# Optimization experiments

Measured on AMD Instinct MI355X. Metric: run time of the kernel, lower is better.

Reference implementation:

```python
import jax, jax.numpy as jnp
import numpy as np

DIM, H, C = 1024, 16, 64
D = DIM // H  # head_dim = 64
GATE_HID = 16


def setup_inputs() -> dict:
    key = jax.random.key(0)
    ks = jax.random.split(key, 8)
    B, L = 2, 2048

    def xav(k, fan_in, fan_out):
        return jax.random.normal(k, (fan_in, fan_out), jnp.float32) * np.sqrt(2.0 / (fan_in + fan_out))

    return {
        "x": jax.random.normal(ks[0], (B, L, DIM), jnp.float32),
        "Wq": xav(ks[1], DIM, DIM), "bq": jnp.zeros((DIM,), jnp.float32),
        "Wk": xav(ks[2], DIM, DIM), "bk": jnp.zeros((DIM,), jnp.float32),
        "Wv": xav(ks[3], DIM, DIM), "bv": jnp.zeros((DIM,), jnp.float32),
        "Wg1": xav(ks[4], DIM, GATE_HID), "bg1": jnp.zeros((GATE_HID,), jnp.float32),
        "Wg2": xav(ks[5], GATE_HID, H * D), "bg2": jnp.zeros((H * D,), jnp.float32),
    }


def reference(x, Wq, bq, Wk, bk, Wv, bv, Wg1, bg1, Wg2, bg2):
    B, L, dim = x.shape
    pad = (-L) % C
    if pad:
        x = jnp.pad(x, ((0, 0), (0, pad), (0, 0)))
    Lp = L + pad

    def proj(W, b):
        # (B, Lp, dim) -> (B, H, Lp, D)
        return (x @ W + b).reshape(B, Lp, H, D).transpose(0, 2, 1, 3)

    q, k, v = proj(Wq, bq), proj(Wk, bk), proj(Wv, bv)
    gate = jax.nn.sigmoid(jax.nn.silu(x @ Wg1 + bg1) @ Wg2 + bg2)
    alpha = 0.9 * gate.reshape(B, Lp, H, D).transpose(0, 2, 1, 3) + 0.1  # (B,H,Lp,D)

    # --- intra-chunk causal softmax attention (vectorized over chunks) ---
    Nc = Lp // C
    qc = q.reshape(B, H, Nc, C, D)
    kc = k.reshape(B, H, Nc, C, D)
    vc = v.reshape(B, H, Nc, C, D)
    scores = jnp.einsum('bhncd,bhnkd->bhnck', qc, kc) / np.sqrt(D).astype(np.float32)
    causal = jnp.tril(jnp.ones((C, C), bool))
    scores = jnp.where(causal, scores, -jnp.inf)
    intra = jnp.einsum('bhnck,bhnke->bhnce', jax.nn.softmax(scores, axis=-1), vc)
    intra = intra.reshape(B, H, Lp, D)

    # --- inter: gated linear-attention recurrence over the full sequence ---
    # Note: in the original code S is updated every timestep (including inside
    # chunks), so the 'inter' term at step t sees ALL tokens < t, not just
    # previous chunks.
    def step(S, inp):
        q_t, k_t, v_t, a_t = inp  # each (B, H, D)
        inter_t = jnp.einsum('bhd,bhde->bhe', q_t, S)
        S = a_t[..., None] * S + k_t[..., None] * v_t[..., None, :]
        return S, inter_t

    xs = tuple(a.transpose(2, 0, 1, 3) for a in (q, k, v, alpha))  # (Lp, B, H, D)
    S0 = jnp.zeros((B, H, D, D), x.dtype)
    _, inter = jax.lax.scan(step, S0, xs)  # (Lp, B, H, D)
    inter = inter.transpose(1, 2, 0, 3)  # (B, H, Lp, D)

    out = (inter + intra).transpose(0, 2, 1, 3).reshape(B, Lp, dim)
    return out[:, :L]
```

## Files before the change

### kernel.cpp

```cpp
#include <hip/hip_runtime.h>
#include <math.h>

#define DIMN 1024
#define NH 16
#define HD 64
#define CHK 64
#define NB 2
#define SEQ 2048
#define NTOK (NB*SEQ)
#define NCHUNK (SEQ/CHK)
#define GH 16

typedef __bf16 bf16x8 __attribute__((ext_vector_type(8)));
typedef float f32x4 __attribute__((ext_vector_type(4)));
typedef unsigned short u16x4 __attribute__((ext_vector_type(4)));

__device__ __forceinline__ unsigned short f2bf(float f) {
  union { float f; unsigned u; } a; a.f = f;
  unsigned r = a.u + 0x7FFFu + ((a.u >> 16) & 1u);
  return (unsigned short)(r >> 16);
}
__device__ __forceinline__ float bf2f(unsigned short v) {
  union { unsigned u; float f; } a; a.u = ((unsigned)v) << 16;
  return a.f;
}

__device__ __forceinline__ void gload16(const void* g, void* l) {
  __builtin_amdgcn_global_load_lds(
      (const __attribute__((address_space(1))) void*)g,
      (__attribute__((address_space(3))) void*)l, 16, 0, 0);
}


__global__ __launch_bounds__(256) void k_cast_x(const float* __restrict__ x,
    unsigned short* __restrict__ xb) {
  size_t i = (size_t)(blockIdx.x*256 + threadIdx.x)*4;
  float4 v = *(const float4*)(x + i);
  ushort4 o;
  o.x = f2bf(v.x); o.y = f2bf(v.y); o.z = f2bf(v.z); o.w = f2bf(v.w);
  *(ushort4*)(xb + i) = o;
}

__global__ __launch_bounds__(256) void k_cast_wT(const float* __restrict__ W0,
    const float* __restrict__ W1, const float* __restrict__ W2,
    unsigned short* __restrict__ wt) {
  __shared__ float tile[64][68];
  int z = blockIdx.z;
  const float* W = z==0 ? W0 : z==1 ? W1 : W2;
  unsigned short* o = wt + (size_t)z*DIMN*DIMN;
  int k0 = blockIdx.y*64, n0 = blockIdx.x*64;
  int tr = threadIdx.x >> 4, c0 = (threadIdx.x & 15)*4;
  #pragma unroll
  for (int s = 0; s < 4; ++s) {
    int r = tr + s*16;
    *(f32x4*)&tile[r][c0] = *(const f32x4*)(W + (size_t)(k0+r)*DIMN + n0 + c0);
  }
  __syncthreads();
  #pragma unroll
  for (int s = 0; s < 4; ++s) {
    int nn = tr + s*16;
    ushort4 v;
    v.x = f2bf(tile[c0+0][nn]);
    v.y = f2bf(tile[c0+1][nn]);
    v.z = f2bf(tile[c0+2][nn]);
    v.w = f2bf(tile[c0+3][nn]);
    *(ushort4*)(o + (size_t)(n0+nn)*DIMN + k0 + c0) = v;
  }
}

__global__ __launch_bounds__(256) void k_wg1t(const float* __restrict__ Wg1,
    unsigned short* __restrict__ wg1b) {
  int idx = blockIdx.x*256 + threadIdx.x;
  int k = idx & 1023, j = idx >> 10;
  wg1b[j*DIMN + k] = f2bf(Wg1[k*GH + j]);
}

__global__ __launch_bounds__(64) void k_hidden(const unsigned short* __restrict__ xb,
    const unsigned short* __restrict__ wg1b, const float* __restrict__ bg1,
    float* __restrict__ hid) {
  int l = threadIdx.x;
  int lr = l & 15, kg = l >> 4;
  int m0 = blockIdx.x * 16;
  union FB { uint4 u; bf16x8 h; } a, b;
  f32x4 acc = {0.f,0.f,0.f,0.f};
  const unsigned short* xrow = xb + (size_t)(m0 + lr)*DIMN + kg*8;
  const unsigned short* wrow = wg1b + (size_t)lr*DIMN + kg*8;
  #pragma unroll 8
  for (int kk = 0; kk < 32; ++kk) {
    a.u = *(const uint4*)(xrow + kk*32);
    b.u = *(const uint4*)(wrow + kk*32);
    acc = __builtin_amdgcn_mfma_f32_16x16x32_bf16(a.h, b.h, acc, 0, 0, 0);
  }
  float bias = bg1[lr];
  #pragma unroll
  for (int rg = 0; rg < 4; ++rg) {
    int m = m0 + kg*4 + rg;
    float v = acc[rg] + bias;
    hid[m*GH + lr] = v / (1.f + expf(-v));
  }
}

__global__ __launch_bounds__(256) void k_projqkv(const unsigned short* __restrict__ xb,
    const unsigned short* __restrict__ wt,
    const float* __restrict__ b0, const float* __restrict__ b1, const float* __restrict__ b2,
    unsigned short* __restrict__ o0, unsigned short* __restrict__ o1,
    unsigned short* __restrict__ o2) {
  __shared__ unsigned short As[2][128*32];
  __shared__ unsigned short Bs[2][128*32];
  int tid = threadIdx.x;
  int n3 = blockIdx.x*128;
  int z = n3 >> 10;
  int n0l = n3 & 1023;
  const float* bias = z==0 ? b0 : z==1 ? b1 : b2;
  unsigned short* out = z==0 ? o0 : z==1 ? o1 : o2;
  int m0 = blockIdx.y*128;

  int l = tid & 63;
  int w = tid >> 6;
  int wr = w >> 1, wc = w & 1;
  int lrow = l & 15, kg = l >> 4;

  f32x4 acc[4][4] = {};

  int r0s = tid >> 2, s0s = tid & 3;
  int r1s = (tid + 256) >> 2;
  int sg0 = s0s ^ ((r0s >> 1) & 3);
  int sg1 = s0s ^ ((r1s >> 1) & 3);

  #define STAGE(buf, kt) do { \
    int kb_ = (kt)*32; \
    gload16(xb + ((size_t)(m0 + r0s)*DIMN + kb_ + sg0*8), &As[buf][tid*8]); \
    gload16(wt + ((size_t)(n3 + r0s)*DIMN + kb_ + sg0*8), &Bs[buf][tid*8]); \
    gload16(xb + ((size_t)(m0 + r1s)*DIMN + kb_ + sg1*8), &As[buf][(tid+256)*8]); \
    gload16(wt + ((size_t)(n3 + r1s)*DIMN + kb_ + sg1*8), &Bs[buf][(tid+256)*8]); \
  } while (0)

  STAGE(0, 0);
  int buf = 0;
  for (int t = 0; t < DIMN/32; ++t) {
    __syncthreads();
    if (t+1 < DIMN/32) STAGE(buf^1, t+1);
    union { uint4 u; bf16x8 h; } af[4], bfr[4];
    #pragma unroll
    for (int mf = 0; mf < 4; ++mf) {
      int r = wr*64 + mf*16 + lrow;
      int slot = kg ^ ((r >> 1) & 3);
      af[mf].u = *(const uint4*)&As[buf][r*32 + slot*8];
    }
    #pragma unroll
    for (int nf = 0; nf < 4; ++nf) {
      int r = wc*64 + nf*16 + lrow;
      int slot = kg ^ ((r >> 1) & 3);
      bfr[nf].u = *(const uint4*)&Bs[buf][r*32 + slot*8];
    }
    #pragma unroll
    for (int mf = 0; mf < 4; ++mf)
      #pragma unroll
      for (int nf = 0; nf < 4; ++nf)
        acc[mf][nf] = __builtin_amdgcn_mfma_f32_16x16x32_bf16(
            af[mf].h, bfr[nf].h, acc[mf][nf], 0, 0, 0);
    buf ^= 1;
  }
  #undef STAGE

  float bv[4];
  #pragma unroll
  for (int nf = 0; nf < 4; ++nf) bv[nf] = bias[n0l + wc*64 + nf*16 + lrow];
  #pragma unroll
  for (int mf = 0; mf < 4; ++mf) {
    int rbase = m0 + wr*64 + mf*16 + kg*4;
    #pragma unroll
    for (int nf = 0; nf < 4; ++nf) {
      int c = n0l + wc*64 + nf*16 + lrow;
      #pragma unroll
      for (int rg = 0; rg < 4; ++rg)
        out[(size_t)(rbase+rg)*DIMN + c] = f2bf(acc[mf][nf][rg] + bv[nf]);
    }
  }
}

__global__ __launch_bounds__(256) void k_ginc(const unsigned short* __restrict__ kbuf,
    const unsigned short* __restrict__ vbuf,
    const float* __restrict__ hid, const float* __restrict__ Wg2,
    const float* __restrict__ bg2,
    float* __restrict__ G, float* __restrict__ Bv) {
  __shared__ __align__(16) float kl[CHK][HD+4];
  __shared__ __align__(16) float vl[CHK][HD+4];
  __shared__ __align__(16) float al[CHK][HD+4];
  __shared__ float wprod[4][HD];
  int tid = threadIdx.x;
  int bid = blockIdx.x;
  int bh = bid >> 5, n = bid & 31;
  int b = bh >> 4, h = bh & 15;
  int colbase = h*HD;
  size_t rowbase = (size_t)b*SEQ + n*CHK;
  int dd = tid & 63, w = tid >> 6;

  float* scr = &al[0][0];
  {
    int r = tid >> 2, j0 = (tid & 3)*4;
    *(f32x4*)&scr[r*16 + j0] = *(const f32x4*)(hid + (rowbase + r)*GH + j0);
    int j = tid >> 4, d0 = (tid & 15)*4;
    *(f32x4*)&scr[1024 + j*64 + d0] = *(const f32x4*)(Wg2 + (size_t)j*DIMN + colbase + d0);
  }
  #pragma unroll
  for (int i = 0; i < 4; ++i) {
    int f4 = tid + i*256;
    int r = f4 >> 4, cg = f4 & 15;
    size_t g = (rowbase + r)*DIMN + colbase + cg*4;
    u16x4 k4 = *(const u16x4*)(kbuf + g);
    u16x4 v4 = *(const u16x4*)(vbuf + g);
    #pragma unroll
    for (int j = 0; j < 4; ++j) {
      kl[r][cg*4+j] = bf2f(k4[j]);
      vl[r][cg*4+j] = bf2f(v4[j]);
    }
  }
  __syncthreads();

  float av[16];
  {
    int r = tid >> 2, db = (tid & 3)*16;
    #pragma unroll
    for (int dq = 0; dq < 16; ++dq) {
      int d = db + dq;
      float acc = bg2[colbase + d];
      #pragma unroll
      for (int j = 0; j < GH; ++j)
        acc = fmaf(scr[r*16 + j], scr[1024 + j*64 + d], acc);
      float gg = 1.f/(1.f + expf(-acc));
      av[dq] = fmaf(0.9f, gg, 0.1f);
    }
  }
  __syncthreads();
  {
    int r = tid >> 2, db = (tid & 3)*16;
    #pragma unroll
    for (int dq = 0; dq < 16; dq += 4) {
      f32x4 v4 = {av[dq], av[dq+1], av[dq+2], av[dq+3]};
      *(f32x4*)&al[r][db + dq] = v4;
    }
  }
  __syncthreads();

  {
    float sp = 1.f;
    for (int ii = 15; ii >= 0; --ii) {
      int i = w*16 + ii;
      kl[i][dd] *= sp;
      sp *= al[i][dd];
    }
    wprod[w][dd] = sp;
  }
  __syncthreads();
  if (w < 3) {
    float tail = 1.f;
    for (int w2 = w+1; w2 < 4; ++w2) tail *= wprod[w2][dd];
    for (int ii = 0; ii < 16; ++ii) kl[w*16+ii][dd] *= tail;
  }
  if (tid < HD)
    Bv[(size_t)bid*HD + tid] = wprod[0][tid]*wprod[1][tid]*wprod[2][tid]*wprod[3][tid];
  __syncthreads();

  int ti = tid >> 4, te = tid & 15;
  int d0 = ti*4, e0 = te*4;
  float acc[4][4] = {};
  for (int i = 0; i < CHK; ++i) {
    float4 kh = *(const float4*)&kl[i][d0];
    float4 vv = *(const float4*)&vl[i][e0];
    float kf[4] = {kh.x,kh.y,kh.z,kh.w};
    float vf[4] = {vv.x,vv.y,vv.z,vv.w};
    #pragma unroll
    for (int r = 0; r < 4; ++r)
      #pragma unroll
      for (int c = 0; c < 4; ++c)
        acc[r][c] = fmaf(kf[r], vf[c], acc[r][c]);
  }
  float* gp = G + (size_t)bid*(HD*HD);
  #pragma unroll
  for (int r = 0; r < 4; ++r) {
    float4 v; v.x=acc[r][0]; v.y=acc[r][1]; v.z=acc[r][2]; v.w=acc[r][3];
    *(float4*)(gp + (d0+r)*HD + e0) = v;
  }
}

__global__ __launch_bounds__(256) void k_scan(const float* __restrict__ buf,
    const float* __restrict__ Bv, unsigned short* __restrict__ stb) {
  int idx = blockIdx.x*256 + threadIdx.x;
  int e = idx & 63, d = (idx >> 6) & 63, bh = idx >> 12;
  const float* gp = buf + (size_t)bh*NCHUNK*HD*HD + d*HD + e;
  unsigned short* sp_ = stb + (size_t)bh*NCHUNK*HD*HD + d*HD + e;
  const float* bp = Bv + (size_t)bh*NCHUNK*HD + d;
  float s = 0.f;
  float g = gp[0], bb = bp[0];
  #pragma unroll
  for (int n = 0; n < NCHUNK; ++n) {
    float gn = 0.f, bn = 0.f;
    if (n+1 < NCHUNK) { gn = gp[(n+1)*(HD*HD)]; bn = bp[(n+1)*HD]; }
    sp_[n*(HD*HD)] = f2bf(s);
    s = fmaf(bb, s, g);
    g = gn; bb = bn;
  }
}

__global__ __launch_bounds__(256) void k_chunk(const unsigned short* __restrict__ qbuf,
    const unsigned short* __restrict__ kbuf, const unsigned short* __restrict__ vbuf,
    const float* __restrict__ hid, const float* __restrict__ Wg2,
    const float* __restrict__ bg2,
    const unsigned short* __restrict__ states, float* __restrict__ outp) {
  __shared__ __align__(16) unsigned short qb16[64*72];
  __shared__ __align__(16) unsigned short kb16[64*72];
  __shared__ __align__(16) unsigned short vT[64*72];
  __shared__ __align__(16) unsigned short Pl[64*72];
  __shared__ __align__(16) unsigned short Swt[2][64*72];
  __shared__ __align__(16) float lb[65*68];
  __shared__ __align__(16) unsigned short dgs[4][16*40];
  __shared__ float seg[4][64];

  const int tid = threadIdx.x;
  const int bid = blockIdx.x;
  const int bh = bid >> 5, n = bid & 31;
  const int b = bh >> 4, h = bh & 15;
  const int colbase = h*HD;
  const size_t rowbase = (size_t)b*SEQ + n*CHK;
  const unsigned short* stp = states + (size_t)(bh*NCHUNK + n)*(HD*HD);

  float* scr = (float*)Pl;
  {
    int r = tid >> 2, j0 = (tid & 3)*4;
    *(f32x4*)&scr[r*16 + j0] = *(const f32x4*)(hid + (rowbase + r)*GH + j0);
    int j = tid >> 4, d0 = (tid & 15)*4;
    *(f32x4*)&scr[1024 + j*64 + d0] = *(const f32x4*)(Wg2 + (size_t)j*DIMN + colbase + d0);
  }
  #pragma unroll
  for (int i = 0; i < 4; ++i) {
    int f4 = tid + i*256;
    int r = f4 >> 4, cg = f4 & 15, c0 = cg*4;
    size_t g = (rowbase + r)*DIMN + colbase + c0;
    u16x4 q4 = *(const u16x4*)(qbuf + g);
    u16x4 k4 = *(const u16x4*)(kbuf + g);
    u16x4 v4 = *(const u16x4*)(vbuf + g);
    u16x4 s4 = *(const u16x4*)(stp + r*HD + c0);
    #pragma unroll
    for (int j = 0; j < 4; ++j) {
      vT[(c0+j)*72 + r] = v4[j];
      Swt[0][(c0+j)*72 + r] = s4[j];
    }
    *(u16x4*)&qb16[r*72 + c0] = q4;
    *(u16x4*)&kb16[r*72 + c0] = k4;
  }
  __syncthreads();

  {
    int r = tid >> 2, db = (tid & 3)*16;
    float av[16];
    #pragma unroll
    for (int dq = 0; dq < 16; ++dq) {
      int d = db + dq;
      float acc = bg2[colbase + d];
      #pragma unroll
      for (int j = 0; j < GH; ++j)
        acc = fmaf(scr[r*16 + j], scr[1024 + j*64 + d], acc);
      float gg = 1.f/(1.f + expf(-acc));
      av[dq] = log2f(fmaf(0.9f, gg, 0.1f));
    }
    #pragma unroll
    for (int dq = 0; dq < 16; dq += 4) {
      f32x4 v4 = {av[dq], av[dq+1], av[dq+2], av[dq+3]};
      *(f32x4*)&lb[r*68 + db + dq] = v4;
    }
  }
  __syncthreads();

  {
    int d = tid & 63, ww = tid >> 6;
    float run = 0.f;
    #pragma unroll
    for (int ii = 0; ii < 16; ++ii) {
      int i = ww*16 + ii;
      float t = lb[i*68 + d];
      lb[i*68 + d] = run;
      run += t;
    }
    seg[ww][d] = run;
  }
  __syncthreads();
  {
    int d = tid & 63, ww = tid >> 6;
    float carry = 0.f;
    for (int w2 = 0; w2 < ww; ++w2) carry += seg[w2][d];
    if (ww > 0)
      for (int ii = 0; ii < 16; ++ii) lb[(ww*16+ii)*68 + d] += carry;
    if (ww == 3) lb[64*68 + d] = carry + seg[3][d];
  }
  __syncthreads();

  const int l = tid & 63, w = tid >> 6;
  const int lr = l & 15, lg = l >> 4;
  const int ks = lg*8;
  const int arow = w*16 + lr;

  union FB { uint4 u; bf16x8 h; unsigned short s[8]; };

  FB qa0, qa1;
  qa0.u = *(const uint4*)&qb16[arow*72 + ks];
  qa1.u = *(const uint4*)&qb16[arow*72 + 32 + ks];
  f32x4 sc[4];
  #pragma unroll
  for (int nf = 0; nf < 4; ++nf) {
    FB b0, b1;
    b0.u = *(const uint4*)&kb16[(nf*16+lr)*72 + ks];
    b1.u = *(const uint4*)&kb16[(nf*16+lr)*72 + 32 + ks];
    f32x4 z = {0.f,0.f,0.f,0.f};
    z = __builtin_amdgcn_mfma_f32_16x16x32_bf16(qa0.h, b0.h, z, 0,0,0);
    z = __builtin_amdgcn_mfma_f32_16x16x32_bf16(qa1.h, b1.h, z, 0,0,0);
    sc[nf] = z;
  }

  float rmax[4] = {-3e38f,-3e38f,-3e38f,-3e38f};
  #pragma unroll
  for (int nf = 0; nf < 4; ++nf) {
    int col = nf*16 + lr;
    #pragma unroll
    for (int rg = 0; rg < 4; ++rg) {
      int row = w*16 + lg*4 + rg;
      float v = sc[nf][rg]*0.125f;
      if (col > row) v = -1e30f;
      sc[nf][rg] = v;
      rmax[rg] = fmaxf(rmax[rg], v);
    }
  }
  #pragma unroll
  for (int m = 1; m <= 8; m <<= 1)
    #pragma unroll
    for (int rg = 0; rg < 4; ++rg)
      rmax[rg] = fmaxf(rmax[rg], __shfl_xor(rmax[rg], m));
  float rsum[4] = {0.f,0.f,0.f,0.f};
  #pragma unroll
  for (int nf = 0; nf < 4; ++nf)
    #pragma unroll
    for (int rg = 0; rg < 4; ++rg) {
      float e = exp2f((sc[nf][rg] - rmax[rg])*1.44269504f);
      sc[nf][rg] = e;
      rsum[rg] += e;
    }
  #pragma unroll
  for (int m = 1; m <= 8; m <<= 1)
    #pragma unroll
    for (int rg = 0; rg < 4; ++rg)
      rsum[rg] += __shfl_xor(rsum[rg], m);
  __syncthreads();
  #pragma unroll
  for (int nf = 0; nf < 4; ++nf)
    #pragma unroll
    for (int rg = 0; rg < 4; ++rg)
      Pl[(w*16 + lg*4 + rg)*72 + nf*16 + lr] = f2bf(sc[nf][rg]);
  float inv[4];
  #pragma unroll
  for (int rg = 0; rg < 4; ++rg) inv[rg] = 1.f/rsum[rg];
  __syncthreads();

  f32x4 acc[4];
  {
    FB p0, p1;
    p0.u = *(const uint4*)&Pl[arow*72 + ks];
    p1.u = *(const uint4*)&Pl[arow*72 + 32 + ks];
    #pragma unroll
    for (int nf = 0; nf < 4; ++nf) {
      FB v0, v1;
      v0.u = *(const uint4*)&vT[(nf*16+lr)*72 + ks];
      v1.u = *(const uint4*)&vT[(nf*16+lr)*72 + 32 + ks];
      f32x4 z = {0.f,0.f,0.f,0.f};
      z = __builtin_amdgcn_mfma_f32_16x16x32_bf16(p0.h, v0.h, z, 0,0,0);
      z = __builtin_amdgcn_mfma_f32_16x16x32_bf16(p1.h, v1.h, z, 0,0,0);
      #pragma unroll
      for (int rg = 0; rg < 4; ++rg)
        acc[nf][rg] = z[rg]*inv[rg];
    }
  }

  {
    int dA = arow;
    float lb32 = lb[32*68 + dA];
    FB ku;
    #pragma unroll
    for (int j = 0; j < 8; ++j) {
      int s = ks + j;
      float kv = bf2f(kb16[s*72 + dA]);
      ku.s[j] = f2bf(kv * exp2f(lb32 - lb[(s+1)*68 + dA]));
    }
    int d0 = w*16 + lg*4;
    float bs[4];
    #pragma unroll
    for (int rg = 0; rg < 4; ++rg) bs[rg] = exp2f(lb[32*68 + d0 + rg]);
    #pragma unroll
    for (int nf = 0; nf < 4; ++nf) {
      int e = nf*16 + lr;
      FB vv;
      vv.u = *(const uint4*)&vT[e*72 + ks];
      f32x4 z = {0.f,0.f,0.f,0.f};
      z = __builtin_amdgcn_mfma_f32_16x16x32_bf16(ku.h, vv.h, z, 0,0,0);
      u16x4 s0v = *(const u16x4*)&Swt[0][e*72 + d0];
      u16x4 s1v;
      #pragma unroll
      for (int rg = 0; rg < 4; ++rg)
        s1v[rg] = f2bf(z[rg] + bs[rg]*bf2f(s0v[rg]));
      *(u16x4*)&Swt[1][e*72 + d0] = s1v;
    }
  }
  __syncthreads();

  {
    const int T = (w >= 2) ? 32 : 0;
    const unsigned short* Ssel = (w >= 2) ? &Swt[1][0] : &Swt[0][0];
    FB qd[2];
    #pragma unroll
    for (int kst = 0; kst < 2; ++kst) {
      int ds = kst*32 + ks;
      f32x4 lbi0 = *(const f32x4*)&lb[arow*68 + ds];
      f32x4 lbi1 = *(const f32x4*)&lb[arow*68 + ds + 4];
      f32x4 lbt0 = *(const f32x4*)&lb[T*68 + ds];
      f32x4 lbt1 = *(const f32x4*)&lb[T*68 + ds + 4];
      FB qr;
      qr.u = *(const uint4*)&qb16[arow*72 + ds];
      #pragma unroll
      for (int j = 0; j < 4; ++j) {
        qd[kst].s[j]   = f2bf(bf2f(qr.s[j])   * exp2f(lbi0[j] - lbt0[j]));
        qd[kst].s[4+j] = f2bf(bf2f(qr.s[4+j]) * exp2f(lbi1[j] - lbt1[j]));
      }
    }
    #pragma unroll
    for (int nf = 0; nf < 4; ++nf) {
      FB s0f, s1f;
      s0f.u = *(const uint4*)&Ssel[(nf*16+lr)*72 + ks];
      s1f.u = *(const uint4*)&Ssel[(nf*16+lr)*72 + 32 + ks];
      acc[nf] = __builtin_amdgcn_mfma_f32_16x16x32_bf16(qd[0].h, s0f.h, acc[nf], 0,0,0);
      acc[nf] = __builtin_amdgcn_mfma_f32_16x16x32_bf16(qd[1].h, s1f.h, acc[nf], 0,0,0);
    }
    const int nb_ = (w & 1) ? 2 : 1;
    f32x4 dgc[2] = {{0.f,0.f,0.f,0.f},{0.f,0.f,0.f,0.f}};
    #pragma unroll
    for (int bf_ = 0; bf_ < 2; ++bf_) {
      if (bf_ < nb_) {
        int s = T + bf_*16 + lr;
        f32x4 z = {0.f,0.f,0.f,0.f};
        #pragma unroll
        for (int kst = 0; kst < 2; ++kst) {
          int ds = kst*32 + ks;
          f32x4 lbt0 = *(const f32x4*)&lb[T*68 + ds];
          f32x4 lbt1 = *(const f32x4*)&lb[T*68 + ds + 4];
          f32x4 lbs0 = *(const f32x4*)&lb[(s+1)*68 + ds];
          f32x4 lbs1 = *(const f32x4*)&lb[(s+1)*68 + ds + 4];
          FB kr, kd;
          kr.u = *(const uint4*)&kb16[s*72 + ds];
          #pragma unroll
          for (int j = 0; j < 4; ++j) {
            kd.s[j]   = f2bf(bf2f(kr.s[j])   * exp2f(lbt0[j] - lbs0[j]));
            kd.s[4+j] = f2bf(bf2f(kr.s[4+j]) * exp2f(lbt1[j] - lbs1[j]));
          }
          z = __builtin_amdgcn_mfma_f32_16x16x32_bf16(qd[kst].h, kd.h, z, 0,0,0);
        }
        dgc[bf_] = z;
      }
    }
    int iis = (w & 1)*16 + lg*4;
    #pragma unroll
    for (int bf_ = 0; bf_ < 2; ++bf_) {
      #pragma unroll
      for (int rg = 0; rg < 4; ++rg) {
        int ssu = bf_*16 + lr;
        float v = (bf_ < nb_ && ssu < iis + rg) ? dgc[bf_][rg] : 0.f;
        dgs[w][(lg*4 + rg)*40 + bf_*16 + lr] = f2bf(v);
      }
    }
    FB dga;
    dga.u = *(const uint4*)&dgs[w][lr*40 + ks];
    #pragma unroll
    for (int nf = 0; nf < 4; ++nf) {
      FB vv;
      vv.u = *(const uint4*)&vT[(nf*16+lr)*72 + T + ks];
      acc[nf] = __builtin_amdgcn_mfma_f32_16x16x32_bf16(dga.h, vv.h, acc[nf], 0,0,0);
    }
  }

  #pragma unroll
  for (int nf = 0; nf < 4; ++nf)
    #pragma unroll
    for (int rg = 0; rg < 4; ++rg)
      outp[(rowbase + w*16 + lg*4 + rg)*DIMN + colbase + nf*16 + lr] = acc[nf][rg];
}

extern "C" void kernel_launch(void* const* d_in, const int* in_sizes, int n_in,
                              void* d_out, int out_size, void* d_ws, size_t ws_size,
                              hipStream_t stream) {
  const float* x   = (const float*)d_in[0];
  const float* Wq  = (const float*)d_in[1];
  const float* bq  = (const float*)d_in[2];
  const float* Wk  = (const float*)d_in[3];
  const float* bk  = (const float*)d_in[4];
  const float* Wv  = (const float*)d_in[5];
  const float* bv  = (const float*)d_in[6];
  const float* Wg1 = (const float*)d_in[7];
  const float* bg1 = (const float*)d_in[8];
  const float* Wg2 = (const float*)d_in[9];
  const float* bg2 = (const float*)d_in[10];
  float* out = (float*)d_out;

  float* ws = (float*)d_ws;
  const size_t NT = (size_t)NTOK*DIMN;
  const size_t NST = (size_t)NB*NH*NCHUNK*HD*HD;
  float* hid = ws;
  float* st  = hid + (size_t)NTOK*GH;
  float* Bv  = st + NST;
  unsigned short* stb = (unsigned short*)(Bv + (size_t)NB*NH*NCHUNK*HD);
  unsigned short* xb = stb + NST;
  unsigned short* wt = xb + NT;
  unsigned short* wg1b = wt + 3*(size_t)DIMN*DIMN;
  unsigned short* qb = wg1b + (size_t)GH*DIMN;
  unsigned short* kb = qb + NT;
  unsigned short* vb = kb + NT;

  k_cast_x<<<NT/(4*256), 256, 0, stream>>>(x, xb);
  k_cast_wT<<<dim3(16, 16, 3), 256, 0, stream>>>(Wq, Wk, Wv, wt);
  k_wg1t<<<(GH*DIMN)/256, 256, 0, stream>>>(Wg1, wg1b);
  k_hidden<<<NTOK/16, 64, 0, stream>>>(xb, wg1b, bg1, hid);
  k_projqkv<<<dim3(3*DIMN/128, NTOK/128), 256, 0, stream>>>(
      xb, wt, bq, bk, bv, qb, kb, vb);
  k_ginc<<<NB*NH*NCHUNK, 256, 0, stream>>>(kb, vb, hid, Wg2, bg2, st, Bv);
  k_scan<<<(NB*NH*HD*HD)/256, 256, 0, stream>>>(st, Bv, stb);
  k_chunk<<<NB*NH*NCHUNK, 256, 0, stream>>>(qb, kb, vb, hid, Wg2, bg2, stb, out);
}
```

Before: 111.0 us.

## Fuse x cast into gate hidden GEMM, swizzle QKV grid, store chunk sums in bf16

Merges the fp32-to-bf16 cast of x into the gate hidden-layer kernel, which now stages 16 rows in LDS and splits K across four waves. This removes one launch and a reread of xb. The QKV projection grid is remapped with a block swizzle to improve L2 reuse. The per-chunk KV outer products are now written in bf16, and the scan overwrites that buffer in place, halving state traffic but adding rounding error before the scan accumulates.

```diff
diff --git a/kernel.cpp b/kernel.cpp
--- a/kernel.cpp
+++ b/kernel.cpp
@@ -31,16 +31,6 @@
       (__attribute__((address_space(3))) void*)l, 16, 0, 0);
 }
 
-
-__global__ __launch_bounds__(256) void k_cast_x(const float* __restrict__ x,
-    unsigned short* __restrict__ xb) {
-  size_t i = (size_t)(blockIdx.x*256 + threadIdx.x)*4;
-  float4 v = *(const float4*)(x + i);
-  ushort4 o;
-  o.x = f2bf(v.x); o.y = f2bf(v.y); o.z = f2bf(v.z); o.w = f2bf(v.w);
-  *(ushort4*)(xb + i) = o;
-}
-
 __global__ __launch_bounds__(256) void k_cast_wT(const float* __restrict__ W0,
     const float* __restrict__ W1, const float* __restrict__ W2,
     unsigned short* __restrict__ wt) {
@@ -75,28 +65,43 @@
   wg1b[j*DIMN + k] = f2bf(Wg1[k*GH + j]);
 }
 
-__global__ __launch_bounds__(64) void k_hidden(const unsigned short* __restrict__ xb,
+__global__ __launch_bounds__(256) void k_castx_hidden(const float* __restrict__ x,
     const unsigned short* __restrict__ wg1b, const float* __restrict__ bg1,
-    float* __restrict__ hid) {
-  int l = threadIdx.x;
+    unsigned short* __restrict__ xb, float* __restrict__ hid) {
+  __shared__ __align__(16) unsigned short xs[16][1032];
+  __shared__ float red[4][16][16];
+  int tid = threadIdx.x;
+  size_t base = (size_t)blockIdx.x * 16 * DIMN;
+  #pragma unroll
+  for (int i = 0; i < 16; ++i) {
+    int idx4 = tid + i*256;
+    int r = idx4 >> 8, c4 = idx4 & 255;
+    f32x4 v = *(const f32x4*)(x + base + (size_t)idx4*4);
+    u16x4 o;
+    o[0]=f2bf(v[0]); o[1]=f2bf(v[1]); o[2]=f2bf(v[2]); o[3]=f2bf(v[3]);
+    *(u16x4*)&xs[r][c4*4] = o;
+    *(u16x4*)(xb + base + (size_t)idx4*4) = o;
+  }
+  __syncthreads();
+  int l = tid & 63, w = tid >> 6;
   int lr = l & 15, kg = l >> 4;
-  int m0 = blockIdx.x * 16;
   union FB { uint4 u; bf16x8 h; } a, b;
   f32x4 acc = {0.f,0.f,0.f,0.f};
-  const unsigned short* xrow = xb + (size_t)(m0 + lr)*DIMN + kg*8;
-  const unsigned short* wrow = wg1b + (size_t)lr*DIMN + kg*8;
-  #pragma unroll 8
-  for (int kk = 0; kk < 32; ++kk) {
-    a.u = *(const uint4*)(xrow + kk*32);
+  const unsigned short* wrow = wg1b + (size_t)lr*DIMN + w*256 + kg*8;
+  #pragma unroll
+  for (int kk = 0; kk < 8; ++kk) {
+    a.u = *(const uint4*)&xs[lr][w*256 + kk*32 + kg*8];
     b.u = *(const uint4*)(wrow + kk*32);
     acc = __builtin_amdgcn_mfma_f32_16x16x32_bf16(a.h, b.h, acc, 0, 0, 0);
   }
-  float bias = bg1[lr];
-  #pragma unroll
-  for (int rg = 0; rg < 4; ++rg) {
-    int m = m0 + kg*4 + rg;
-    float v = acc[rg] + bias;
-    hid[m*GH + lr] = v / (1.f + expf(-v));
+  #pragma unroll
+  for (int rg = 0; rg < 4; ++rg) red[w][kg*4 + rg][lr] = acc[rg];
+  __syncthreads();
+  {
+    int m = tid >> 4, j = tid & 15;
+    float s = red[0][m][j] + red[1][m][j] + red[2][m][j] + red[3][m][j];
+    s += bg1[j];
+    hid[(blockIdx.x*16 + m)*GH + j] = s / (1.f + expf(-s));
   }
 }
 
@@ -108,12 +113,15 @@
   __shared__ unsigned short As[2][128*32];
   __shared__ unsigned short Bs[2][128*32];
   int tid = threadIdx.x;
-  int n3 = blockIdx.x*128;
+  int wg = blockIdx.y * gridDim.x + blockIdx.x;
+  int swz = (wg & 7) * 96 + (wg >> 3);
+  int bx = swz % 24, by = swz / 24;
+  int n3 = bx*128;
   int z = n3 >> 10;
   int n0l = n3 & 1023;
   const float* bias = z==0 ? b0 : z==1 ? b1 : b2;
   unsigned short* out = z==0 ? o0 : z==1 ? o1 : o2;
-  int m0 = blockIdx.y*128;
+  int m0 = by*128;
 
   int l = tid & 63;
   int w = tid >> 6;
@@ -183,7 +191,7 @@
     const unsigned short* __restrict__ vbuf,
     const float* __restrict__ hid, const float* __restrict__ Wg2,
     const float* __restrict__ bg2,
-    float* __restrict__ G, float* __restrict__ Bv) {
+    unsigned short* __restrict__ G, float* __restrict__ Bv) {
   __shared__ __align__(16) float kl[CHK][HD+4];
   __shared__ __align__(16) float vl[CHK][HD+4];
   __shared__ __align__(16) float al[CHK][HD+4];
@@ -276,28 +284,29 @@
       for (int c = 0; c < 4; ++c)
         acc[r][c] = fmaf(kf[r], vf[c], acc[r][c]);
   }
-  float* gp = G + (size_t)bid*(HD*HD);
+  unsigned short* gp = G + (size_t)bid*(HD*HD);
   #pragma unroll
   for (int r = 0; r < 4; ++r) {
-    float4 v; v.x=acc[r][0]; v.y=acc[r][1]; v.z=acc[r][2]; v.w=acc[r][3];
-    *(float4*)(gp + (d0+r)*HD + e0) = v;
-  }
-}
-
-__global__ __launch_bounds__(256) void k_scan(const float* __restrict__ buf,
-    const float* __restrict__ Bv, unsigned short* __restrict__ stb) {
+    ushort4 o;
+    o.x = f2bf(acc[r][0]); o.y = f2bf(acc[r][1]);
+    o.z = f2bf(acc[r][2]); o.w = f2bf(acc[r][3]);
+    *(ushort4*)(gp + (d0+r)*HD + e0) = o;
+  }
+}
+
+__global__ __launch_bounds__(256) void k_scan(unsigned short* __restrict__ buf,
+    const float* __restrict__ Bv) {
   int idx = blockIdx.x*256 + threadIdx.x;
   int e = idx & 63, d = (idx >> 6) & 63, bh = idx >> 12;
-  const float* gp = buf + (size_t)bh*NCHUNK*HD*HD + d*HD + e;
-  unsigned short* sp_ = stb + (size_t)bh*NCHUNK*HD*HD + d*HD + e;
+  unsigned short* gp = buf + (size_t)bh*NCHUNK*HD*HD + d*HD + e;
   const float* bp = Bv + (size_t)bh*NCHUNK*HD + d;
   float s = 0.f;
-  float g = gp[0], bb = bp[0];
+  float g = bf2f(gp[0]), bb = bp[0];
   #pragma unroll
   for (int n = 0; n < NCHUNK; ++n) {
     float gn = 0.f, bn = 0.f;
-    if (n+1 < NCHUNK) { gn = gp[(n+1)*(HD*HD)]; bn = bp[(n+1)*HD]; }
-    sp_[n*(HD*HD)] = f2bf(s);
+    if (n+1 < NCHUNK) { gn = bf2f(gp[(n+1)*(HD*HD)]); bn = bp[(n+1)*HD]; }
+    gp[n*(HD*HD)] = f2bf(s);
     s = fmaf(bb, s, g);
     g = gn; bb = bn;
   }
@@ -610,8 +619,7 @@
   const size_t NT = (size_t)NTOK*DIMN;
   const size_t NST = (size_t)NB*NH*NCHUNK*HD*HD;
   float* hid = ws;
-  float* st  = hid + (size_t)NTOK*GH;
-  float* Bv  = st + NST;
+  float* Bv  = hid + (size_t)NTOK*GH;
   unsigned short* stb = (unsigned short*)(Bv + (size_t)NB*NH*NCHUNK*HD);
   unsigned short* xb = stb + NST;
   unsigned short* wt = xb + NT;
@@ -620,13 +628,12 @@
   unsigned short* kb = qb + NT;
   unsigned short* vb = kb + NT;
 
-  k_cast_x<<<NT/(4*256), 256, 0, stream>>>(x, xb);
   k_cast_wT<<<dim3(16, 16, 3), 256, 0, stream>>>(Wq, Wk, Wv, wt);
   k_wg1t<<<(GH*DIMN)/256, 256, 0, stream>>>(Wg1, wg1b);
-  k_hidden<<<NTOK/16, 64, 0, stream>>>(xb, wg1b, bg1, hid);
-  k_projqkv<<<dim3(3*DIMN/128, NTOK/128), 256, 0, stream>>>(
+  k_castx_hidden<<<NTOK/16, 256, 0, stream>>>(x, wg1b, bg1, xb, hid);
+  k_projqkv<<<dim3(24, 32), 256, 0, stream>>>(
       xb, wt, bq, bk, bv, qb, kb, vb);
-  k_ginc<<<NB*NH*NCHUNK, 256, 0, stream>>>(kb, vb, hid, Wg2, bg2, st, Bv);
-  k_scan<<<(NB*NH*HD*HD)/256, 256, 0, stream>>>(st, Bv, stb);
+  k_ginc<<<NB*NH*NCHUNK, 256, 0, stream>>>(kb, vb, hid, Wg2, bg2, stb, Bv);
+  k_scan<<<(NB*NH*HD*HD)/256, 256, 0, stream>>>(stb, Bv);
   k_chunk<<<NB*NH*NCHUNK, 256, 0, stream>>>(qb, kb, vb, hid, Wg2, bg2, stb, out);
 }
```

New measurement: 105.6 us. 4.8% less time.
